# Kernel tuning notes

Hardware: AMD Instinct MI355X
Metric: run time of the kernel (lower is better)

Reference implementation:

```python
import jax, jax.numpy as jnp
import numpy as np

LN_EPS = 1e-5


def setup_inputs() -> dict:
    key = jax.random.key(0)
    k1, k2, k3 = jax.random.split(key, 3)
    B, C, N, T, K = 8, 64, 512, 288, 32
    x = jax.random.normal(k1, (B, C, N, T), dtype=jnp.float32)
    HEs = jax.random.uniform(k2, (N, K), dtype=jnp.float32)  # relu(tanh(...)) in [0,1)
    edge_map = jax.random.normal(k3, (K, K), dtype=jnp.float32) / np.sqrt(K)
    return {"x": x, "HEs": HEs, "edge_map": edge_map}


def reference(x, HEs, edge_map):
    # x: [B, C, N, T]; HEs: [N, K]; edge_map: [K, K]
    B, C, N, T = x.shape
    xt = jnp.transpose(x, (0, 3, 2, 1))            # [B, T, N, C]
    feat = xt.reshape(B * T, N, C)                 # [B*T, N, C]
    # hyperedge aggregation: HEs^T @ feat
    hyper_feat = jnp.einsum('nk,bnc->bkc', HEs, feat)          # [B*T, K, C]
    hyper_mapped = jax.nn.relu(jnp.einsum('kj,bjc->bkc', edge_map, hyper_feat))
    hyper_out = hyper_mapped + hyper_feat
    # scatter back to nodes
    y = jax.nn.relu(jnp.einsum('nk,bkc->bnc', HEs, hyper_out)) # [B*T, N, C]
    y = y.reshape(B, T, N, C)
    z = y + xt
    # fresh LayerNorm over last dim (C), affine params are identity (ones/zeros)
    mu = jnp.mean(z, axis=-1, keepdims=True)
    var = jnp.mean(jnp.square(z - mu), axis=-1, keepdims=True)
    z = (z - mu) * jax.lax.rsqrt(var + LN_EPS)
    return jnp.transpose(z, (0, 3, 2, 1))          # [B, C, N, T]
```

## Files before the change

### kernel.cpp

```cpp
#include <hip/hip_runtime.h>

#define B_ 8
#define C_ 64
#define N_ 512
#define T_ 288
#define K_ 32

typedef __bf16 bf16;
typedef __attribute__((ext_vector_type(4))) __bf16 bf16x4;
typedef __attribute__((ext_vector_type(8))) __bf16 bf16x8;
typedef __attribute__((ext_vector_type(4))) float f32x4;

__global__ __launch_bounds__(256) void k_prep(const void* __restrict__ x,
                                              const void* __restrict__ hes,
                                              const void* __restrict__ em,
                                              bf16* __restrict__ hesb,
                                              bf16* __restrict__ hest,
                                              bf16* __restrict__ emb,
                                              int* __restrict__ flag) {
    __shared__ float sm[256];
    const bf16* xb = (const bf16*)x;
    float m = 0.f;
    for (int i = threadIdx.x; i < 4096; i += 256) {
        float a = fabsf((float)xb[i]);
        if (!(a <= 1000.f)) a = 1e30f;
        m = fmaxf(m, a);
    }
    sm[threadIdx.x] = m;
    __syncthreads();
    for (int s = 128; s > 0; s >>= 1) {
        if (threadIdx.x < s) sm[threadIdx.x] = fmaxf(sm[threadIdx.x], sm[threadIdx.x + s]);
        __syncthreads();
    }
    const int f32 = (sm[0] > 1000.f) ? 1 : 0;
    if (blockIdx.x == 0 && threadIdx.x == 0) *flag = f32;

    int idx = blockIdx.x * 256 + threadIdx.x;
    if (idx < N_ * K_) {
        float v = f32 ? ((const float*)hes)[idx] : (float)((const bf16*)hes)[idx];
        hesb[idx] = (bf16)v;
        int n = idx >> 5, k = idx & 31;
        hest[k * N_ + n] = (bf16)v;
    }
    if (idx < K_ * K_) {
        float v = f32 ? ((const float*)em)[idx] : (float)((const bf16*)em)[idx];
        emb[idx] = (bf16)v;
    }
}

template <int F32>
__device__ __forceinline__ void hyper_body(const void* __restrict__ x,
                                           const bf16* __restrict__ hest,
                                           const bf16* __restrict__ emb,
                                           bf16* __restrict__ ho) {
    const int tile = blockIdx.x, c = blockIdx.y, b = blockIdx.z;
    const int lane = threadIdx.x;
    const int col  = lane & 15;
    const int q    = lane >> 4;
    const int t0   = tile * 32;
    const size_t xbase = ((size_t)(b * C_ + c)) * N_ * T_;

    __shared__ bf16  xT[32][136];
    __shared__ float hf[K_][33];

    const int tq = lane & 7;
    const int rw = lane >> 3;

    f32x4 acc[2][2] = {};
    for (int chunk = 0; chunk < 4; ++chunk) {
        const int nc = chunk * 128;
        #pragma unroll
        for (int it = 0; it < 16; ++it) {
            const int row = it * 8 + rw;
            const size_t gi = xbase + (size_t)(nc + row) * T_ + t0 + 4 * tq;
            float v0, v1, v2, v3;
            if (F32) {
                f32x4 v = *(const f32x4*)((const float*)x + gi);
                v0 = v[0]; v1 = v[1]; v2 = v[2]; v3 = v[3];
            } else {
                bf16x4 v = *(const bf16x4*)((const bf16*)x + gi);
                v0 = (float)v[0]; v1 = (float)v[1]; v2 = (float)v[2]; v3 = (float)v[3];
            }
            xT[4 * tq + 0][row] = (bf16)v0;
            xT[4 * tq + 1][row] = (bf16)v1;
            xT[4 * tq + 2][row] = (bf16)v2;
            xT[4 * tq + 3][row] = (bf16)v3;
        }
        __syncthreads();
        #pragma unroll
        for (int s = 0; s < 4; ++s) {
            const int nl = s * 32;
            const int ng = nc + nl;
            bf16x8 a0 = *(const bf16x8*)(hest + (size_t)(col) * N_ + ng + 8 * q);
            bf16x8 a1 = *(const bf16x8*)(hest + (size_t)(16 + col) * N_ + ng + 8 * q);
            bf16x8 b0 = *(const bf16x8*)(&xT[col][nl + 8 * q]);
            bf16x8 b1 = *(const bf16x8*)(&xT[16 + col][nl + 8 * q]);
            acc[0][0] = __builtin_amdgcn_mfma_f32_16x16x32_bf16(a0, b0, acc[0][0], 0, 0, 0);
            acc[0][1] = __builtin_amdgcn_mfma_f32_16x16x32_bf16(a0, b1, acc[0][1], 0, 0, 0);
            acc[1][0] = __builtin_amdgcn_mfma_f32_16x16x32_bf16(a1, b0, acc[1][0], 0, 0, 0);
            acc[1][1] = __builtin_amdgcn_mfma_f32_16x16x32_bf16(a1, b1, acc[1][1], 0, 0, 0);
        }
        __syncthreads();
    }

    #pragma unroll
    for (int mt = 0; mt < 2; ++mt)
        #pragma unroll
        for (int tt = 0; tt < 2; ++tt)
            #pragma unroll
            for (int r = 0; r < 4; ++r)
                hf[16 * mt + 4 * q + r][16 * tt + col] = acc[mt][tt][r];
    __syncthreads();

    f32x4 acc2[2][2];
    #pragma unroll
    for (int mt = 0; mt < 2; ++mt) {
        bf16x8 a = *(const bf16x8*)(emb + (size_t)(16 * mt + col) * K_ + 8 * q);
        #pragma unroll
        for (int tt = 0; tt < 2; ++tt) {
            bf16x8 bb;
            #pragma unroll
            for (int jj = 0; jj < 8; ++jj)
                bb[jj] = (bf16)hf[8 * q + jj][16 * tt + col];
            f32x4 zero = {};
            acc2[mt][tt] = __builtin_amdgcn_mfma_f32_16x16x32_bf16(a, bb, zero, 0, 0, 0);
        }
    }

    #pragma unroll
    for (int mt = 0; mt < 2; ++mt)
        #pragma unroll
        for (int tt = 0; tt < 2; ++tt) {
            bf16x4 v;
            #pragma unroll
            for (int r = 0; r < 4; ++r) {
                float hv = acc2[mt][tt][r];
                hv = hv > 0.f ? hv : 0.f;
                hv += acc[mt][tt][r];
                v[r] = (bf16)hv;
            }
            *(bf16x4*)(ho + (((size_t)(b * C_ + c)) * T_ + t0 + 16 * tt + col) * K_
                          + 16 * mt + 4 * q) = v;
        }
}

__global__ __launch_bounds__(64, 3) void k_hyper(const void* __restrict__ x,
                                                 const int* __restrict__ flag,
                                                 const bf16* __restrict__ hest,
                                                 const bf16* __restrict__ emb,
                                                 bf16* __restrict__ ho) {
    if (*flag) hyper_body<1>(x, hest, emb, ho);
    else       hyper_body<0>(x, hest, emb, ho);
}

template <int F32>
__device__ __forceinline__ void scatter_body(const void* __restrict__ x,
                                             const bf16* __restrict__ hesb,
                                             const bf16* __restrict__ ho,
                                             void* __restrict__ outp) {
    const int wg  = blockIdx.x;
    const int b   = wg & 7;
    const int pos = wg >> 3;
    const int bx  = pos % 9;
    const int n0  = (pos / 9) * 16;

    const int tid   = threadIdx.x;
    const int w     = tid >> 6;
    const int lane  = tid & 63;
    const int col   = lane & 15;
    const int q     = lane >> 4;
    const int thalf = w & 1;
    const int cgrp  = w >> 1;
    const int t0    = bx * 32 + thalf * 16;

    bf16x8 hb = *(const bf16x8*)(hesb + (size_t)(n0 + col) * K_ + 8 * q);

    f32x4 z[16];
    float s1[4] = {0.f, 0.f, 0.f, 0.f}, s2[4] = {0.f, 0.f, 0.f, 0.f};
    const bf16* hob = ho + (((size_t)(b * C_)) * T_ + t0 + col) * K_ + 8 * q;
    const size_t xb = ((size_t)b * C_) * (size_t)N_ * T_;
    #pragma unroll
    for (int i = 0; i < 16; ++i) {
        const int c = cgrp * 16 + i;
        bf16x8 a = *(const bf16x8*)(hob + (size_t)c * T_ * K_);
        f32x4 zero = {};
        f32x4 zz = __builtin_amdgcn_mfma_f32_16x16x32_bf16(a, hb, zero, 0, 0, 0);
        const size_t xi = xb + ((size_t)c * N_ + n0 + col) * T_ + t0 + 4 * q;
        f32x4 xv;
        if (F32) {
            xv = *(const f32x4*)((const float*)x + xi);
        } else {
            bf16x4 x4 = *(const bf16x4*)((const bf16*)x + xi);
            xv[0] = (float)x4[0]; xv[1] = (float)x4[1];
            xv[2] = (float)x4[2]; xv[3] = (float)x4[3];
        }
        #pragma unroll
        for (int r = 0; r < 4; ++r) {
            float v = zz[r];
            v = v > 0.f ? v : 0.f;
            v += xv[r];
            zz[r] = v;
            s1[r] += v;
            s2[r] += v * v;
        }
        z[i] = zz;
    }

    __shared__ float sh1[2][4][16][17];
    __shared__ float sh2[2][4][16][17];
    #pragma unroll
    for (int r = 0; r < 4; ++r) {
        sh1[thalf][cgrp][4 * q + r][col] = s1[r];
        sh2[thalf][cgrp][4 * q + r][col] = s2[r];
    }
    __syncthreads();

    {
        const int th = tid >> 8, rr = (tid >> 4) & 15, cc = tid & 15;
        float S1 = sh1[th][0][rr][cc] + sh1[th][1][rr][cc]
                 + sh1[th][2][rr][cc] + sh1[th][3][rr][cc];
        float S2 = sh2[th][0][rr][cc] + sh2[th][1][rr][cc]
                 + sh2[th][2][rr][cc] + sh2[th][3][rr][cc];
        float mu  = S1 * (1.f / 64.f);
        float var = S2 * (1.f / 64.f) - mu * mu;
        float rs  = rsqrtf(var + 1e-5f);
        sh1[th][0][rr][cc] = mu;
        sh2[th][0][rr][cc] = rs;
    }
    __syncthreads();

    float mu_r[4], rs_r[4];
    #pragma unroll
    for (int r = 0; r < 4; ++r) {
        mu_r[r] = sh1[thalf][0][4 * q + r][col];
        rs_r[r] = sh2[thalf][0][4 * q + r][col];
    }
    #pragma unroll
    for (int i = 0; i < 16; ++i) {
        const int c = cgrp * 16 + i;
        const size_t oi = ((size_t)(b * C_ + c) * N_ + n0 + col) * T_ + t0 + 4 * q;
        if (F32) {
            f32x4 v;
            #pragma unroll
            for (int r = 0; r < 4; ++r) v[r] = (z[i][r] - mu_r[r]) * rs_r[r];
            *(f32x4*)((float*)outp + oi) = v;
        } else {
            bf16x4 v;
            #pragma unroll
            for (int r = 0; r < 4; ++r) v[r] = (bf16)((z[i][r] - mu_r[r]) * rs_r[r]);
            *(bf16x4*)((bf16*)outp + oi) = v;
        }
    }
}

__global__ __launch_bounds__(512, 2) void k_scatter_ln(const void* __restrict__ x,
                                                       const int* __restrict__ flag,
                                                       const bf16* __restrict__ hesb,
                                                       const bf16* __restrict__ ho,
                                                       void* __restrict__ outp) {
    if (*flag) scatter_body<1>(x, hesb, ho, outp);
    else       scatter_body<0>(x, hesb, ho, outp);
}

extern "C" void kernel_launch(void* const* d_in, const int* in_sizes, int n_in,
                              void* d_out, int out_size, void* d_ws, size_t ws_size,
                              hipStream_t stream) {
    const void* x   = d_in[0];
    const void* hes = d_in[1];
    const void* em  = d_in[2];

    char* ws = (char*)d_ws;
    int*  flag = (int*)ws;
    bf16* hesb = (bf16*)(ws + 64);
    bf16* hest = hesb + (size_t)N_ * K_;
    bf16* emb  = hest + (size_t)K_ * N_;
    bf16* ho   = emb  + (size_t)K_ * K_;

    k_prep<<<dim3((N_ * K_ + 255) / 256), 256, 0, stream>>>(x, hes, em, hesb, hest, emb, flag);
    k_hyper<<<dim3(T_ / 32, C_, B_), 64, 0, stream>>>(x, flag, hest, emb, ho);
    k_scatter_ln<<<dim3((T_ / 32) * (N_ / 16) * B_, 1, 1), 512, 0, stream>>>(x, flag, hesb, ho, d_out);
}
```

Measured before the change: 603.1 us.

## Retile scatter-LN to 16-wide time tiles, 8 warps over channels, nontemporal IO

The scatter/LayerNorm kernel now gives each workgroup a 16x16 (node, time) tile, with its 8 waves each covering 8 channels. This halves per-thread register arrays and doubles the number of workgroups. x loads and output stores use nontemporal hints to avoid polluting cache with streamed data. The hyper kernel also aliases its xT and hf shared buffers to cut LDS use. The trade-offs are shorter 32-byte contiguous time segments per row and a larger cross-wave reduction.

New measurement: 627.8 us. 4.1% more time.

```diff
diff --git a/kernel.cpp b/kernel.cpp
--- a/kernel.cpp
+++ b/kernel.cpp
@@ -60,8 +60,9 @@
     const int t0   = tile * 32;
     const size_t xbase = ((size_t)(b * C_ + c)) * N_ * T_;
 
-    __shared__ bf16  xT[32][136];
-    __shared__ float hf[K_][33];
+    __shared__ char smraw[32 * 136 * sizeof(bf16)];
+    bf16 (*xT)[136] = (bf16(*)[136])smraw;
+    float (*hf)[33] = (float(*)[33])smraw;
 
     const int tq = lane & 7;
     const int rw = lane >> 3;
@@ -90,9 +91,9 @@
         #pragma unroll
         for (int s = 0; s < 4; ++s) {
             const int nl = s * 32;
-            const int ng = nc + nl;
-            bf16x8 a0 = *(const bf16x8*)(hest + (size_t)(col) * N_ + ng + 8 * q);
-            bf16x8 a1 = *(const bf16x8*)(hest + (size_t)(16 + col) * N_ + ng + 8 * q);
+            const int ng2 = nc + nl;
+            bf16x8 a0 = *(const bf16x8*)(hest + (size_t)(col) * N_ + ng2 + 8 * q);
+            bf16x8 a1 = *(const bf16x8*)(hest + (size_t)(16 + col) * N_ + ng2 + 8 * q);
             bf16x8 b0 = *(const bf16x8*)(&xT[col][nl + 8 * q]);
             bf16x8 b1 = *(const bf16x8*)(&xT[16 + col][nl + 8 * q]);
             acc[0][0] = __builtin_amdgcn_mfma_f32_16x16x32_bf16(a0, b0, acc[0][0], 0, 0, 0);
@@ -161,36 +162,34 @@
     const int wg  = blockIdx.x;
     const int b   = wg & 7;
     const int pos = wg >> 3;
-    const int bx  = pos % 9;
-    const int n0  = (pos / 9) * 16;
-
-    const int tid   = threadIdx.x;
-    const int w     = tid >> 6;
-    const int lane  = tid & 63;
-    const int col   = lane & 15;
-    const int q     = lane >> 4;
-    const int thalf = w & 1;
-    const int cgrp  = w >> 1;
-    const int t0    = bx * 32 + thalf * 16;
+    const int bx  = pos % 18;
+    const int n0  = (pos / 18) * 16;
+
+    const int tid  = threadIdx.x;
+    const int w    = tid >> 6;
+    const int lane = tid & 63;
+    const int col  = lane & 15;
+    const int q    = lane >> 4;
+    const int t0   = bx * 16;
 
     bf16x8 hb = *(const bf16x8*)(hesb + (size_t)(n0 + col) * K_ + 8 * q);
 
-    f32x4 z[16];
+    f32x4 z[8];
     float s1[4] = {0.f, 0.f, 0.f, 0.f}, s2[4] = {0.f, 0.f, 0.f, 0.f};
     const bf16* hob = ho + (((size_t)(b * C_)) * T_ + t0 + col) * K_ + 8 * q;
     const size_t xb = ((size_t)b * C_) * (size_t)N_ * T_;
     #pragma unroll
-    for (int i = 0; i < 16; ++i) {
-        const int c = cgrp * 16 + i;
+    for (int i = 0; i < 8; ++i) {
+        const int c = w * 8 + i;
         bf16x8 a = *(const bf16x8*)(hob + (size_t)c * T_ * K_);
         f32x4 zero = {};
         f32x4 zz = __builtin_amdgcn_mfma_f32_16x16x32_bf16(a, hb, zero, 0, 0, 0);
         const size_t xi = xb + ((size_t)c * N_ + n0 + col) * T_ + t0 + 4 * q;
         f32x4 xv;
         if (F32) {
-            xv = *(const f32x4*)((const float*)x + xi);
+            xv = __builtin_nontemporal_load((const f32x4*)((const float*)x + xi));
         } else {
-            bf16x4 x4 = *(const bf16x4*)((const bf16*)x + xi);
+            bf16x4 x4 = __builtin_nontemporal_load((const bf16x4*)((const bf16*)x + xi));
             xv[0] = (float)x4[0]; xv[1] = (float)x4[1];
             xv[2] = (float)x4[2]; xv[3] = (float)x4[3];
         }
@@ -206,49 +205,51 @@
         z[i] = zz;
     }
 
-    __shared__ float sh1[2][4][16][17];
-    __shared__ float sh2[2][4][16][17];
+    __shared__ float sh1[8][16][17];
+    __shared__ float sh2[8][16][17];
     #pragma unroll
     for (int r = 0; r < 4; ++r) {
-        sh1[thalf][cgrp][4 * q + r][col] = s1[r];
-        sh2[thalf][cgrp][4 * q + r][col] = s2[r];
-    }
-    __syncthreads();
-
-    {
-        const int th = tid >> 8, rr = (tid >> 4) & 15, cc = tid & 15;
-        float S1 = sh1[th][0][rr][cc] + sh1[th][1][rr][cc]
-                 + sh1[th][2][rr][cc] + sh1[th][3][rr][cc];
-        float S2 = sh2[th][0][rr][cc] + sh2[th][1][rr][cc]
-                 + sh2[th][2][rr][cc] + sh2[th][3][rr][cc];
+        sh1[w][4 * q + r][col] = s1[r];
+        sh2[w][4 * q + r][col] = s2[r];
+    }
+    __syncthreads();
+
+    if (tid < 256) {
+        const int rr = tid >> 4, cc = tid & 15;
+        float S1 = 0.f, S2 = 0.f;
+        #pragma unroll
+        for (int g = 0; g < 8; ++g) {
+            S1 += sh1[g][rr][cc];
+            S2 += sh2[g][rr][cc];
+        }
         float mu  = S1 * (1.f / 64.f);
         float var = S2 * (1.f / 64.f) - mu * mu;
         float rs  = rsqrtf(var + 1e-5f);
-        sh1[th][0][rr][cc] = mu;
-        sh2[th][0][rr][cc] = rs;
+        sh1[0][rr][cc] = mu;
+        sh2[0][rr][cc] = rs;
     }
     __syncthreads();
 
     float mu_r[4], rs_r[4];
     #pragma unroll
     for (int r = 0; r < 4; ++r) {
-        mu_r[r] = sh1[thalf][0][4 * q + r][col];
-        rs_r[r] = sh2[thalf][0][4 * q + r][col];
-    }
-    #pragma unroll
-    for (int i = 0; i < 16; ++i) {
-        const int c = cgrp * 16 + i;
+        mu_r[r] = sh1[0][4 * q + r][col];
+        rs_r[r] = sh2[0][4 * q + r][col];
+    }
+    #pragma unroll
+    for (int i = 0; i < 8; ++i) {
+        const int c = w * 8 + i;
         const size_t oi = ((size_t)(b * C_ + c) * N_ + n0 + col) * T_ + t0 + 4 * q;
         if (F32) {
             f32x4 v;
             #pragma unroll
             for (int r = 0; r < 4; ++r) v[r] = (z[i][r] - mu_r[r]) * rs_r[r];
-            *(f32x4*)((float*)outp + oi) = v;
+            __builtin_nontemporal_store(v, (f32x4*)((float*)outp + oi));
         } else {
             bf16x4 v;
             #pragma unroll
             for (int r = 0; r < 4; ++r) v[r] = (bf16)((z[i][r] - mu_r[r]) * rs_r[r]);
-            *(bf16x4*)((bf16*)outp + oi) = v;
+            __builtin_nontemporal_store(v, (bf16x4*)((bf16*)outp + oi));
         }
     }
 }
@@ -278,5 +279,5 @@
 
     k_prep<<<dim3((N_ * K_ + 255) / 256), 256, 0, stream>>>(x, hes, em, hesb, hest, emb, flag);
     k_hyper<<<dim3(T_ / 32, C_, B_), 64, 0, stream>>>(x, flag, hest, emb, ho);
-    k_scatter_ln<<<dim3((T_ / 32) * (N_ / 16) * B_, 1, 1), 512, 0, stream>>>(x, flag, hesb, ho, d_out);
-}
+    k_scatter_ln<<<dim3((T_ / 16) * (N_ / 16) * B_, 1, 1), 512, 0, stream>>>(x, flag, hesb, ho, d_out);
+}
```
